# Kernel tuning notes

Measured on AMD Instinct MI355X. Metric: run time of the kernel, lower is better.

## Reference

```python
import math
import jax, jax.numpy as jnp
import numpy as np

B, T, D, H = 1, 4096, 1024, 16
HD = D // H  # 64

def setup_inputs() -> dict:
    key = jax.random.key(0)
    k1, k2, k3 = jax.random.split(key, 3)
    x = jax.random.normal(k1, (B, T, D), dtype=jnp.float32)
    # torch nn.Linear weight layout: [out_features, in_features]
    w_attn = jax.random.normal(k2, (3 * D, D), dtype=jnp.float32) * (1.0 / math.sqrt(D))
    w_proj = jax.random.normal(k3, (D, D), dtype=jnp.float32) * (1.0 / math.sqrt(D))
    return {"x": x, "w_attn": w_attn, "w_proj": w_proj}

def reference(x, w_attn, w_proj):
    b, t, d = x.shape
    qkv = jnp.einsum('btd,ed->bte', x, w_attn)  # [B,T,3D]
    q, k, v = jnp.split(qkv, 3, axis=-1)
    # [B,H,T,HD]
    q = q.reshape(b, t, H, HD).transpose(0, 2, 1, 3)
    k = k.reshape(b, t, H, HD).transpose(0, 2, 1, 3)
    v = v.reshape(b, t, H, HD).transpose(0, 2, 1, 3)
    scale = 1.0 / math.sqrt(HD)
    att = jnp.einsum('bhqd,bhkd->bhqk', q, k) * scale  # [B,H,T,T]
    causal = jnp.tril(jnp.ones((t, t), dtype=bool))
    att = jnp.where(causal[None, None], att, -jnp.inf)
    att = jax.nn.softmax(att, axis=-1)
    y = jnp.einsum('bhqk,bhkd->bhqd', att, v)  # [B,H,T,HD]
    y = y.transpose(0, 2, 1, 3).reshape(b, t, d)
    return jnp.einsum('btd,ed->bte', y, w_proj)
```

## Files before the change

kernel.cpp:

```cpp
#include <hip/hip_runtime.h>
#include <hip/hip_bf16.h>

typedef __bf16 bf16x8 __attribute__((ext_vector_type(8)));
typedef float  f32x4  __attribute__((ext_vector_type(4)));
typedef short  sh4    __attribute__((ext_vector_type(4)));

__device__ __forceinline__ void async_load16(const void* g, void* l) {
    __builtin_amdgcn_global_load_lds(
        (const __attribute__((address_space(1))) unsigned int*)g,
        (__attribute__((address_space(3))) unsigned int*)l,
        16, 0, 0);
}

__device__ __forceinline__ bool sniff_is_bf16(const void* src) {
    const unsigned int* p = (const unsigned int*)src;
    unsigned v = p[threadIdx.x & 63];
    unsigned e = (v >> 7) & 0xFF;
    unsigned long long m = __ballot(e >= 100 && e <= 140);
    return __popcll(m) >= 48;
}

__global__ __launch_bounds__(256) void to_bf16(const void* __restrict__ src,
                                               __bf16* __restrict__ dst, int n) {
    bool b16 = sniff_is_bf16(src);
    int i = (blockIdx.x * 256 + threadIdx.x) * 4;
    if (i >= n) return;
    if (b16) {
        *(uint2*)(dst + i) = *(const uint2*)((const __bf16*)src + i);
    } else {
        float4 v = *(const float4*)((const float*)src + i);
        dst[i]     = (__bf16)v.x;
        dst[i + 1] = (__bf16)v.y;
        dst[i + 2] = (__bf16)v.z;
        dst[i + 3] = (__bf16)v.w;
    }
}

__global__ __launch_bounds__(256) void gemm_bt(
    const __bf16* __restrict__ A,
    const __bf16* __restrict__ B,
    void* __restrict__ Cv,
    int M, int N, int K,
    const void* sniff)
{
    bool out_b16 = true;
    if (sniff) out_b16 = sniff_is_bf16(sniff);

    __shared__ __bf16 As[128 * 32];
    __shared__ __bf16 Bs[128 * 32];

    const int tid  = threadIdx.x;
    const int lane = tid & 63;
    const int w    = tid >> 6;
    const int wm   = w >> 1, wn = w & 1;
    const int m0   = blockIdx.y * 128;
    const int n0   = blockIdx.x * 128;
    const int c    = lane & 15;
    const int g    = lane >> 4;

    f32x4 acc[4][4] = {};

    const int e0 = tid * 8;
    const int e1 = e0 + 2048;
    const int r0 = e0 >> 5, c0 = e0 & 31;
    const int r1 = e1 >> 5, c1 = e1 & 31;

    for (int k0 = 0; k0 < K; k0 += 32) {
        async_load16(A + (size_t)(m0 + r0) * K + k0 + c0, As + e0);
        async_load16(A + (size_t)(m0 + r1) * K + k0 + c1, As + e1);
        async_load16(B + (size_t)(n0 + r0) * K + k0 + c0, Bs + e0);
        async_load16(B + (size_t)(n0 + r1) * K + k0 + c1, Bs + e1);
        __syncthreads();

        bf16x8 af[4], bfr[4];
        #pragma unroll
        for (int i = 0; i < 4; i++)
            af[i] = *(const bf16x8*)&As[(wm * 64 + i * 16 + c) * 32 + g * 8];
        #pragma unroll
        for (int j = 0; j < 4; j++)
            bfr[j] = *(const bf16x8*)&Bs[(wn * 64 + j * 16 + c) * 32 + g * 8];
        #pragma unroll
        for (int i = 0; i < 4; i++)
            #pragma unroll
            for (int j = 0; j < 4; j++)
                acc[i][j] = __builtin_amdgcn_mfma_f32_16x16x32_bf16(af[i], bfr[j], acc[i][j], 0, 0, 0);
        __syncthreads();
    }

    #pragma unroll
    for (int i = 0; i < 4; i++) {
        const int row0 = m0 + wm * 64 + i * 16 + g * 4;
        #pragma unroll
        for (int j = 0; j < 4; j++) {
            const int col = n0 + wn * 64 + j * 16 + c;
            #pragma unroll
            for (int r = 0; r < 4; r++) {
                const size_t idx = (size_t)(row0 + r) * N + col;
                if (out_b16) ((__bf16*)Cv)[idx] = (__bf16)acc[i][j][r];
                else         ((float*)Cv)[idx]  = acc[i][j][r];
            }
        }
    }
}

__global__ __launch_bounds__(256) void vtrans(const __bf16* __restrict__ qkv,
                                              __bf16* __restrict__ vT) {
    __shared__ __bf16 Lt[64 * 72];
    const int tid = threadIdx.x;
    const int h   = blockIdx.y;
    const int t0  = blockIdx.x * 64;
    #pragma unroll
    for (int rr = 0; rr < 2; rr++) {
        int e = rr * 2048 + tid * 8;
        int tr = e >> 6, tc = e & 63;
        bf16x8 v = *(const bf16x8*)&qkv[(size_t)(t0 + tr) * 3072 + 2048 + h * 64 + tc];
        #pragma unroll
        for (int i = 0; i < 8; i++) Lt[(tc + i) * 72 + tr] = v[i];
    }
    __syncthreads();
    #pragma unroll
    for (int rr = 0; rr < 2; rr++) {
        int e = rr * 2048 + tid * 8;
        int dr = e >> 6, dc = e & 63;
        *(bf16x8*)&vT[(size_t)h * 262144 + (size_t)dr * 4096 + t0 + dc]
            = *(const bf16x8*)&Lt[dr * 72 + dc];
    }
}

__global__ __launch_bounds__(256) void attn_fwd(
    const __bf16* __restrict__ qkv,
    const __bf16* __restrict__ vT,
    __bf16* __restrict__ y)
{
    constexpr int LDQ = 3072;
    constexpr float SCL = 0.18033688011112042f;
    constexpr float MEXP = 16.0f;

    __shared__ __align__(16) char raw[50176];
    __bf16* ksb = (__bf16*)raw;
    __bf16* vsb = (__bf16*)(raw + 24576);
    float*  ls  = (float*)(raw + 49152);
    float*  F   = (float*)raw;

    const int id   = blockIdx.x;
    const int h    = (id & 7) * 2 + (id >> 8);
    const int pr   = (id >> 3) & 31;
    const int tid  = threadIdx.x;
    const int lane = tid & 63;
    const int w    = tid >> 6;
    const int c    = lane & 15;
    const int g    = lane >> 4;
    const int qoff = h * 64;

    const int p0 = tid, p1 = tid + 256;
    const int sr0 = p0 >> 3, sg0 = ((p0 & 7) ^ (sr0 & 7)) * 8;
    const int sr1 = p1 >> 3, sg1 = ((p1 & 7) ^ (sr1 & 7)) * 8;
    const __bf16* vbase = vT + (size_t)h * 262144;

    const int qts[2] = {63 - pr, pr};

    #pragma unroll 1
    for (int ph = 0; ph < 2; ph++) {
        const int qt  = qts[ph];
        const int qs  = qt * 64;
        const int nkt = qt + 1;

        __syncthreads();

        {
            async_load16(qkv + (size_t)sr0 * LDQ + 1024 + qoff + sg0, ksb + p0 * 8);
            async_load16(qkv + (size_t)sr1 * LDQ + 1024 + qoff + sg1, ksb + p1 * 8);
            async_load16(vbase + (size_t)sr0 * 4096 + sg0, vsb + p0 * 8);
            async_load16(vbase + (size_t)sr1 * 4096 + sg1, vsb + p1 * 8);
            if (nkt > 1) {
                async_load16(qkv + (size_t)(64 + sr0) * LDQ + 1024 + qoff + sg0, ksb + 4096 + p0 * 8);
                async_load16(qkv + (size_t)(64 + sr1) * LDQ + 1024 + qoff + sg1, ksb + 4096 + p1 * 8);
                async_load16(vbase + (size_t)sr0 * 4096 + 64 + sg0, vsb + 4096 + p0 * 8);
                async_load16(vbase + (size_t)sr1 * 4096 + 64 + sg1, vsb + 4096 + p1 * 8);
            }
        }

        bf16x8 qf[4][2];
        #pragma unroll
        for (int n = 0; n < 4; n++) {
            const __bf16* qrow = qkv + (size_t)(qs + n * 16 + c) * LDQ + qoff;
            bf16x8 q0 = *(const bf16x8*)(qrow + g * 8);
            bf16x8 q1 = *(const bf16x8*)(qrow + 32 + g * 8);
            #pragma unroll
            for (int i = 0; i < 8; i++) {
                qf[n][0][i] = (__bf16)((float)q0[i] * SCL);
                qf[n][1][i] = (__bf16)((float)q1[i] * SCL);
            }
        }

        float l_lane[4] = {};
        f32x4 o[4][4] = {};

        for (int t = 0; t < nkt; t++) {
            if (t + 1 < nkt) asm volatile("s_waitcnt vmcnt(4)" ::: "memory");
            else             asm volatile("s_waitcnt vmcnt(0)" ::: "memory");
            __builtin_amdgcn_s_barrier();
            asm volatile("" ::: "memory");

            if (t + 2 < nkt) {
                const int nks = (t + 2) * 64;
                const int nb  = (t + 2) % 3;
                async_load16(qkv + (size_t)(nks + sr0) * LDQ + 1024 + qoff + sg0, ksb + (nb * 4096 + p0 * 8));
                async_load16(qkv + (size_t)(nks + sr1) * LDQ + 1024 + qoff + sg1, ksb + (nb * 4096 + p1 * 8));
                async_load16(vbase + (size_t)sr0 * 4096 + nks + sg0, vsb + (nb * 4096 + p0 * 8));
                async_load16(vbase + (size_t)sr1 * 4096 + nks + sg1, vsb + (nb * 4096 + p1 * 8));
            }

            const __bf16* ks_ = ksb + (t % 3) * 4096;
            const __bf16* vs_ = vsb + (t % 3) * 4096;

            f32x4 sa[4] = {};
            #pragma unroll
            for (int s = 0; s < 2; s++) {
                bf16x8 kf = *(const bf16x8*)&ks_[(w * 16 + c) * 64 + ((s * 4 + g) ^ (c & 7)) * 8];
                #pragma unroll
                for (int n = 0; n < 4; n++)
                    sa[n] = __builtin_amdgcn_mfma_f32_16x16x32_bf16(kf, qf[n][s], sa[n], 0, 0, 0);
            }

            if (t == nkt - 1) {
                #pragma unroll
                for (int n = 0; n < 4; n++)
                    #pragma unroll
                    for (int r = 0; r < 4; r++)
                        if (w * 16 + g * 4 + r > n * 16 + c) sa[n][r] = -1e30f;
            }

            sh4 vf[4];
            #pragma unroll
            for (int j = 0; j < 4; j++)
                vf[j] = *(const sh4*)&vs_[(j * 16 + c) * 64 + ((2 * w + (g >> 1)) ^ (c & 7)) * 8 + (g & 1) * 4];

            #pragma unroll
            for (int n = 0; n < 4; n++) {
                __bf16 pb[4] __attribute__((aligned(8)));
                #pragma unroll
                for (int r = 0; r < 4; r++) {
                    float p = __builtin_amdgcn_exp2f(sa[n][r] - MEXP);
                    l_lane[n] += p;
                    pb[r] = (__bf16)p;
                }
                sh4 pbs = *(const sh4*)pb;
                #pragma unroll
                for (int j = 0; j < 4; j++)
                    o[j][n] = __builtin_amdgcn_mfma_f32_16x16x16bf16_1k(vf[j], pbs, o[j][n], 0, 0, 0);
            }
        }

        #pragma unroll
        for (int n = 0; n < 4; n++) {
            l_lane[n] += __shfl_xor(l_lane[n], 16);
            l_lane[n] += __shfl_xor(l_lane[n], 32);
        }
        __syncthreads();
        if (g == 0) {
            #pragma unroll
            for (int n = 0; n < 4; n++) ls[(w * 4 + n) * 16 + c] = l_lane[n];
        }
        __syncthreads();
        float l_run = ls[(0 * 4 + w) * 16 + c] + ls[(1 * 4 + w) * 16 + c]
                    + ls[(2 * 4 + w) * 16 + c] + ls[(3 * 4 + w) * 16 + c];
        const float rl = 1.0f / l_run;

        #pragma unroll
        for (int j = 0; j < 4; j++) {
            __syncthreads();
            #pragma unroll
            for (int n = 0; n < 4; n++)
                *(f32x4*)&F[((w * 64) + (n * 16 + c)) * 20 + g * 4] = o[j][n];
            __syncthreads();
            f32x4 t0 = *(const f32x4*)&F[((0 * 64) + (w * 16 + c)) * 20 + g * 4];
            f32x4 t1 = *(const f32x4*)&F[((1 * 64) + (w * 16 + c)) * 20 + g * 4];
            f32x4 t2 = *(const f32x4*)&F[((2 * 64) + (w * 16 + c)) * 20 + g * 4];
            f32x4 t3 = *(const f32x4*)&F[((3 * 64) + (w * 16 + c)) * 20 + g * 4];
            f32x4 tt = t0 + t1 + t2 + t3;
            __bf16 ob[4] __attribute__((aligned(8)));
            #pragma unroll
            for (int r = 0; r < 4; r++) ob[r] = (__bf16)(tt[r] * rl);
            *(uint2*)&y[(size_t)(qs + w * 16 + c) * 1024 + qoff + j * 16 + g * 4]
                = *(const uint2*)ob;
        }
    }
}

extern "C" void kernel_launch(void* const* d_in, const int* in_sizes, int n_in,
                              void* d_out, int out_size, void* d_ws, size_t ws_size,
                              hipStream_t stream) {
    constexpr int T = 4096, D = 1024;

    __bf16* cx   = (__bf16*)d_ws;
    __bf16* cwa  = cx  + (size_t)T * D;
    __bf16* cwp  = cwa + (size_t)3 * D * D;
    __bf16* qkv  = cwp + (size_t)D * D;
    __bf16* y    = qkv + (size_t)T * 3 * D;
    __bf16* vT   = cx;

    to_bf16<<<T * D / 1024, 256, 0, stream>>>(d_in[0], cx, T * D);
    to_bf16<<<3 * D * D / 1024, 256, 0, stream>>>(d_in[1], cwa, 3 * D * D);
    to_bf16<<<D * D / 1024, 256, 0, stream>>>(d_in[2], cwp, D * D);

    gemm_bt<<<dim3(3 * D / 128, T / 128), 256, 0, stream>>>(cx, cwa, qkv, T, 3 * D, D, nullptr);
    vtrans<<<dim3(T / 64, 16), 256, 0, stream>>>(qkv, vT);
    attn_fwd<<<512, 256, 0, stream>>>(qkv, vT, y);
    gemm_bt<<<dim3(D / 128, T / 128), 256, 0, stream>>>(y, cwp, d_out, T, D, D, d_in[2]);
}
```

Baseline: 222.3 us.

## Split attention query tile across 8 waves and remap GEMM blocks per XCD

The attention kernel now runs 512 threads per block. Each of 8 waves handles one 16-key slice and one 32-query half, which halves per-wave accumulator registers and doubles the waves available to hide latency. Each thread issues half as many async tile loads, and the waitcnt is adjusted to match. The GEMM launch becomes a 1D grid whose block IDs are remapped so consecutive tiles land on the same XCD, for better L2 locality. The risks are extra barrier cost with more waves, half the waves sitting idle during the epilogue, and a remap that assumes the grid size divides by 8.

```diff
diff --git a/kernel.cpp b/kernel.cpp
--- a/kernel.cpp
+++ b/kernel.cpp
@@ -49,12 +49,19 @@
     __shared__ __bf16 As[128 * 32];
     __shared__ __bf16 Bs[128 * 32];
 
+    const int nwg = gridDim.x;
+    const int cpx = nwg >> 3;
+    const int sid = (blockIdx.x & 7) * cpx + (blockIdx.x >> 3);
+    const int nbx = N >> 7;
+    const int bx  = sid % nbx;
+    const int by  = sid / nbx;
+
     const int tid  = threadIdx.x;
     const int lane = tid & 63;
     const int w    = tid >> 6;
     const int wm   = w >> 1, wn = w & 1;
-    const int m0   = blockIdx.y * 128;
-    const int n0   = blockIdx.x * 128;
+    const int m0   = by * 128;
+    const int n0   = bx * 128;
     const int c    = lane & 15;
     const int g    = lane >> 4;
 
@@ -127,7 +134,7 @@
     }
 }
 
-__global__ __launch_bounds__(256) void attn_fwd(
+__global__ __launch_bounds__(512, 4) void attn_fwd(
     const __bf16* __restrict__ qkv,
     const __bf16* __restrict__ vT,
     __bf16* __restrict__ y)
@@ -148,13 +155,13 @@
     const int tid  = threadIdx.x;
     const int lane = tid & 63;
     const int w    = tid >> 6;
+    const int kw   = w & 3;
+    const int qw   = w >> 2;
     const int c    = lane & 15;
     const int g    = lane >> 4;
     const int qoff = h * 64;
 
-    const int p0 = tid, p1 = tid + 256;
-    const int sr0 = p0 >> 3, sg0 = ((p0 & 7) ^ (sr0 & 7)) * 8;
-    const int sr1 = p1 >> 3, sg1 = ((p1 & 7) ^ (sr1 & 7)) * 8;
+    const int sr = tid >> 3, sg = ((tid & 7) ^ (sr & 7)) * 8;
     const __bf16* vbase = vT + (size_t)h * 262144;
 
     const int qts[2] = {63 - pr, pr};
@@ -167,23 +174,17 @@
 
         __syncthreads();
 
-        {
-            async_load16(qkv + (size_t)sr0 * LDQ + 1024 + qoff + sg0, ksb + p0 * 8);
-            async_load16(qkv + (size_t)sr1 * LDQ + 1024 + qoff + sg1, ksb + p1 * 8);
-            async_load16(vbase + (size_t)sr0 * 4096 + sg0, vsb + p0 * 8);
-            async_load16(vbase + (size_t)sr1 * 4096 + sg1, vsb + p1 * 8);
-            if (nkt > 1) {
-                async_load16(qkv + (size_t)(64 + sr0) * LDQ + 1024 + qoff + sg0, ksb + 4096 + p0 * 8);
-                async_load16(qkv + (size_t)(64 + sr1) * LDQ + 1024 + qoff + sg1, ksb + 4096 + p1 * 8);
-                async_load16(vbase + (size_t)sr0 * 4096 + 64 + sg0, vsb + 4096 + p0 * 8);
-                async_load16(vbase + (size_t)sr1 * 4096 + 64 + sg1, vsb + 4096 + p1 * 8);
-            }
-        }
-
-        bf16x8 qf[4][2];
-        #pragma unroll
-        for (int n = 0; n < 4; n++) {
-            const __bf16* qrow = qkv + (size_t)(qs + n * 16 + c) * LDQ + qoff;
+        async_load16(qkv + (size_t)sr * LDQ + 1024 + qoff + sg, ksb + tid * 8);
+        async_load16(vbase + (size_t)sr * 4096 + sg, vsb + tid * 8);
+        if (nkt > 1) {
+            async_load16(qkv + (size_t)(64 + sr) * LDQ + 1024 + qoff + sg, ksb + 4096 + tid * 8);
+            async_load16(vbase + (size_t)sr * 4096 + 64 + sg, vsb + 4096 + tid * 8);
+        }
+
+        bf16x8 qf[2][2];
+        #pragma unroll
+        for (int n = 0; n < 2; n++) {
+            const __bf16* qrow = qkv + (size_t)(qs + qw * 32 + n * 16 + c) * LDQ + qoff;
             bf16x8 q0 = *(const bf16x8*)(qrow + g * 8);
             bf16x8 q1 = *(const bf16x8*)(qrow + 32 + g * 8);
             #pragma unroll
@@ -193,11 +194,11 @@
             }
         }
 
-        float l_lane[4] = {};
-        f32x4 o[4][4] = {};
+        float l_lane[2] = {};
+        f32x4 o[4][2] = {};
 
         for (int t = 0; t < nkt; t++) {
-            if (t + 1 < nkt) asm volatile("s_waitcnt vmcnt(4)" ::: "memory");
+            if (t + 1 < nkt) asm volatile("s_waitcnt vmcnt(2)" ::: "memory");
             else             asm volatile("s_waitcnt vmcnt(0)" ::: "memory");
             __builtin_amdgcn_s_barrier();
             asm volatile("" ::: "memory");
@@ -205,39 +206,37 @@
             if (t + 2 < nkt) {
                 const int nks = (t + 2) * 64;
                 const int nb  = (t + 2) % 3;
-                async_load16(qkv + (size_t)(nks + sr0) * LDQ + 1024 + qoff + sg0, ksb + (nb * 4096 + p0 * 8));
-                async_load16(qkv + (size_t)(nks + sr1) * LDQ + 1024 + qoff + sg1, ksb + (nb * 4096 + p1 * 8));
-                async_load16(vbase + (size_t)sr0 * 4096 + nks + sg0, vsb + (nb * 4096 + p0 * 8));
-                async_load16(vbase + (size_t)sr1 * 4096 + nks + sg1, vsb + (nb * 4096 + p1 * 8));
+                async_load16(qkv + (size_t)(nks + sr) * LDQ + 1024 + qoff + sg, ksb + (nb * 4096 + tid * 8));
+                async_load16(vbase + (size_t)sr * 4096 + nks + sg, vsb + (nb * 4096 + tid * 8));
             }
 
             const __bf16* ks_ = ksb + (t % 3) * 4096;
             const __bf16* vs_ = vsb + (t % 3) * 4096;
 
-            f32x4 sa[4] = {};
+            f32x4 sa[2] = {};
             #pragma unroll
             for (int s = 0; s < 2; s++) {
-                bf16x8 kf = *(const bf16x8*)&ks_[(w * 16 + c) * 64 + ((s * 4 + g) ^ (c & 7)) * 8];
-                #pragma unroll
-                for (int n = 0; n < 4; n++)
+                bf16x8 kf = *(const bf16x8*)&ks_[(kw * 16 + c) * 64 + ((s * 4 + g) ^ (c & 7)) * 8];
+                #pragma unroll
+                for (int n = 0; n < 2; n++)
                     sa[n] = __builtin_amdgcn_mfma_f32_16x16x32_bf16(kf, qf[n][s], sa[n], 0, 0, 0);
             }
 
             if (t == nkt - 1) {
                 #pragma unroll
-                for (int n = 0; n < 4; n++)
+                for (int n = 0; n < 2; n++)
                     #pragma unroll
                     for (int r = 0; r < 4; r++)
-                        if (w * 16 + g * 4 + r > n * 16 + c) sa[n][r] = -1e30f;
+                        if (kw * 16 + g * 4 + r > qw * 32 + n * 16 + c) sa[n][r] = -1e30f;
             }
 
             sh4 vf[4];
             #pragma unroll
             for (int j = 0; j < 4; j++)
-                vf[j] = *(const sh4*)&vs_[(j * 16 + c) * 64 + ((2 * w + (g >> 1)) ^ (c & 7)) * 8 + (g & 1) * 4];
-
-            #pragma unroll
-            for (int n = 0; n < 4; n++) {
+                vf[j] = *(const sh4*)&vs_[(j * 16 + c) * 64 + ((2 * kw + (g >> 1)) ^ (c & 7)) * 8 + (g & 1) * 4];
+
+            #pragma unroll
+            for (int n = 0; n < 2; n++) {
                 __bf16 pb[4] __attribute__((aligned(8)));
                 #pragma unroll
                 for (int r = 0; r < 4; r++) {
@@ -253,37 +252,42 @@
         }
 
         #pragma unroll
-        for (int n = 0; n < 4; n++) {
+        for (int n = 0; n < 2; n++) {
             l_lane[n] += __shfl_xor(l_lane[n], 16);
             l_lane[n] += __shfl_xor(l_lane[n], 32);
         }
         __syncthreads();
         if (g == 0) {
             #pragma unroll
-            for (int n = 0; n < 4; n++) ls[(w * 4 + n) * 16 + c] = l_lane[n];
-        }
-        __syncthreads();
-        float l_run = ls[(0 * 4 + w) * 16 + c] + ls[(1 * 4 + w) * 16 + c]
-                    + ls[(2 * 4 + w) * 16 + c] + ls[(3 * 4 + w) * 16 + c];
-        const float rl = 1.0f / l_run;
+            for (int n = 0; n < 2; n++) ls[(kw * 4 + qw * 2 + n) * 16 + c] = l_lane[n];
+        }
+        __syncthreads();
+        float rl = 0.f;
+        if (w < 4) {
+            float l_run = ls[(0 * 4 + w) * 16 + c] + ls[(1 * 4 + w) * 16 + c]
+                        + ls[(2 * 4 + w) * 16 + c] + ls[(3 * 4 + w) * 16 + c];
+            rl = 1.0f / l_run;
+        }
 
         #pragma unroll
         for (int j = 0; j < 4; j++) {
             __syncthreads();
             #pragma unroll
-            for (int n = 0; n < 4; n++)
-                *(f32x4*)&F[((w * 64) + (n * 16 + c)) * 20 + g * 4] = o[j][n];
+            for (int n = 0; n < 2; n++)
+                *(f32x4*)&F[((kw * 64) + (qw * 32 + n * 16 + c)) * 20 + g * 4] = o[j][n];
             __syncthreads();
-            f32x4 t0 = *(const f32x4*)&F[((0 * 64) + (w * 16 + c)) * 20 + g * 4];
-            f32x4 t1 = *(const f32x4*)&F[((1 * 64) + (w * 16 + c)) * 20 + g * 4];
-            f32x4 t2 = *(const f32x4*)&F[((2 * 64) + (w * 16 + c)) * 20 + g * 4];
-            f32x4 t3 = *(const f32x4*)&F[((3 * 64) + (w * 16 + c)) * 20 + g * 4];
-            f32x4 tt = t0 + t1 + t2 + t3;
-            __bf16 ob[4] __attribute__((aligned(8)));
-            #pragma unroll
-            for (int r = 0; r < 4; r++) ob[r] = (__bf16)(tt[r] * rl);
-            *(uint2*)&y[(size_t)(qs + w * 16 + c) * 1024 + qoff + j * 16 + g * 4]
-                = *(const uint2*)ob;
+            if (w < 4) {
+                f32x4 t0 = *(const f32x4*)&F[((0 * 64) + (w * 16 + c)) * 20 + g * 4];
+                f32x4 t1 = *(const f32x4*)&F[((1 * 64) + (w * 16 + c)) * 20 + g * 4];
+                f32x4 t2 = *(const f32x4*)&F[((2 * 64) + (w * 16 + c)) * 20 + g * 4];
+                f32x4 t3 = *(const f32x4*)&F[((3 * 64) + (w * 16 + c)) * 20 + g * 4];
+                f32x4 tt = t0 + t1 + t2 + t3;
+                __bf16 ob[4] __attribute__((aligned(8)));
+                #pragma unroll
+                for (int r = 0; r < 4; r++) ob[r] = (__bf16)(tt[r] * rl);
+                *(uint2*)&y[(size_t)(qs + w * 16 + c) * 1024 + qoff + j * 16 + g * 4]
+                    = *(const uint2*)ob;
+            }
         }
     }
 }
@@ -304,8 +308,8 @@
     to_bf16<<<3 * D * D / 1024, 256, 0, stream>>>(d_in[1], cwa, 3 * D * D);
     to_bf16<<<D * D / 1024, 256, 0, stream>>>(d_in[2], cwp, D * D);
 
-    gemm_bt<<<dim3(3 * D / 128, T / 128), 256, 0, stream>>>(cx, cwa, qkv, T, 3 * D, D, nullptr);
+    gemm_bt<<<(3 * D / 128) * (T / 128), 256, 0, stream>>>(cx, cwa, qkv, T, 3 * D, D, nullptr);
     vtrans<<<dim3(T / 64, 16), 256, 0, stream>>>(qkv, vT);
-    attn_fwd<<<512, 256, 0, stream>>>(qkv, vT, y);
-    gemm_bt<<<dim3(D / 128, T / 128), 256, 0, stream>>>(y, cwp, d_out, T, D, D, d_in[2]);
-}
+    attn_fwd<<<512, 512, 0, stream>>>(qkv, vT, y);
+    gemm_bt<<<(D / 128) * (T / 128), 256, 0, stream>>>(y, cwp, d_out, T, D, D, d_in[2]);
+}
```

Result: faster. 211.3 us (-5.0%).
